# Performance work log

Hardware: AMD Instinct MI355X
Metric: run time of the kernel (lower is better)

The kernel has to match this reference:

```python
import jax, jax.numpy as jnp
import numpy as np

B, G, C = 16384, 7, 30  # batch, 7x7 grid, 2*5 box params + 20 classes


def setup_inputs() -> dict:
    key = jax.random.key(0)
    k1, k2 = jax.random.split(key)
    pred = jax.random.uniform(k1, (B, G, G, C), dtype=jnp.float32)
    labels = jax.random.uniform(k2, (B, G, G, C), dtype=jnp.float32)
    # channel 0 of labels is the object-presence indicator (==1 where a gt box exists)
    labels = labels.at[..., 0].set((labels[..., 0] > 0.7).astype(jnp.float32))
    return {"pred": pred, "labels": labels}


def _corners(box):
    # box channels: [conf, x, y, w, h]
    x, y, w, h = box[..., 1], box[..., 2], box[..., 3], box[..., 4]
    return x - 0.5 * w, x + 0.5 * w, y - 0.5 * h, y + 0.5 * h  # left,right,top,bottom


def _iou(b1, b2):
    l1, r1, t1, bt1 = _corners(b1)
    l2, r2, t2, bt2 = _corners(b2)
    in_h = jnp.minimum(bt1, bt2) - jnp.maximum(t1, t2)
    in_w = jnp.minimum(r1, r2) - jnp.maximum(l1, l2)
    inter = jnp.where((in_h < 0) | (in_w < 0), 0.0, in_h * in_w)
    area1 = (bt1 - t1) * (r1 - l1)
    area2 = (bt2 - t2) * (r2 - l2)
    return inter / (area1 + area2 - inter)


def reference(pred, labels):
    mask = labels[..., 0]                     # [B,7,7] object indicator (0/1)
    box1 = pred[..., 0:5]
    box2 = pred[..., 5:10]
    gt = labels[..., 0:5]
    iou1 = _iou(box1, gt)
    iou2 = _iou(box2, gt)
    best = iou1 >= iou2                       # responsible box per cell
    sel = jnp.where(best[..., None], box1, box2)
    iou_max = jnp.where(best, iou1, iou2)
    iou_min = jnp.where(best, iou2, iou1)
    center = 5.0 * ((sel[..., 1] - gt[..., 1]) ** 2 + (sel[..., 2] - gt[..., 2]) ** 2)
    wh = 5.0 * ((jnp.sqrt(sel[..., 3]) - jnp.sqrt(gt[..., 3])) ** 2
                + (jnp.sqrt(sel[..., 4]) - jnp.sqrt(gt[..., 4])) ** 2)
    cls = jnp.sum((pred[..., 10:] - labels[..., 10:]) ** 2, axis=-1)

    def msum(x):
        return jnp.sum(x * mask)

    # [center, wh, obj_conf, noobj_conf, classification]
    return jnp.stack([msum(center), msum(wh), msum(iou_max), msum(iou_min), msum(cls)])
```

## Files before the change

kernel.cpp:

```cpp
#include <hip/hip_runtime.h>

#define NCH 30
#define CPB 256
#define TPB 256

__device__ __forceinline__ float iou_f(float x1, float y1, float w1, float h1,
                                       float x2, float y2, float w2, float h2) {
    float l1 = x1 - 0.5f * w1, r1 = x1 + 0.5f * w1;
    float t1 = y1 - 0.5f * h1, b1 = y1 + 0.5f * h1;
    float l2 = x2 - 0.5f * w2, r2 = x2 + 0.5f * w2;
    float t2 = y2 - 0.5f * h2, b2 = y2 + 0.5f * h2;
    float in_h = fminf(b1, b2) - fmaxf(t1, t2);
    float in_w = fminf(r1, r2) - fmaxf(l1, l2);
    float inter = (in_h < 0.f || in_w < 0.f) ? 0.f : in_h * in_w;
    float a1 = (b1 - t1) * (r1 - l1);
    float a2 = (b2 - t2) * (r2 - l2);
    return inter / (a1 + a2 - inter);
}

__global__ __launch_bounds__(TPB) void yolo_loss(const float* __restrict__ pred,
                                                 const float* __restrict__ lab,
                                                 float* __restrict__ out,
                                                 int n_cells) {
    __shared__ float s_p[CPB * NCH];
    __shared__ float s_l[CPB * NCH];
    __shared__ float red[5][TPB / 64];

    const int tid = threadIdx.x;
    const size_t cell0 = (size_t)blockIdx.x * CPB;
    const size_t base = cell0 * NCH;
    const size_t total = (size_t)n_cells * NCH;

    const float4* gp = (const float4*)(pred + base);
    const float4* gl = (const float4*)(lab + base);
    float4* sp = (float4*)s_p;
    float4* sl = (float4*)s_l;
    const int nvec = CPB * NCH / 4;
    const size_t avail = (total > base) ? (total - base) : 0;
    const int nv = (int)((avail / 4) < (size_t)nvec ? (avail / 4) : (size_t)nvec);
    for (int i = tid; i < nv; i += TPB) {
        sp[i] = gp[i];
        sl[i] = gl[i];
    }
    __syncthreads();

    float v0 = 0.f, v1 = 0.f, v2 = 0.f, v3 = 0.f, v4 = 0.f;
    if (cell0 + (size_t)tid < (size_t)n_cells) {
        const float* cp = s_p + tid * NCH;
        const float* cl = s_l + tid * NCH;
        float mask = cl[0];
        float gx = cl[1], gy = cl[2], gw = cl[3], gh = cl[4];

        float i1 = iou_f(cp[1], cp[2], cp[3], cp[4], gx, gy, gw, gh);
        float i2 = iou_f(cp[6], cp[7], cp[8], cp[9], gx, gy, gw, gh);
        bool best = (i1 >= i2);
        float sx = best ? cp[1] : cp[6];
        float sy = best ? cp[2] : cp[7];
        float sw = best ? cp[3] : cp[8];
        float sh = best ? cp[4] : cp[9];
        float imax = best ? i1 : i2;
        float imin = best ? i2 : i1;

        float center = 5.f * ((sx - gx) * (sx - gx) + (sy - gy) * (sy - gy));
        float dw = sqrtf(sw) - sqrtf(gw);
        float dh = sqrtf(sh) - sqrtf(gh);
        float wh = 5.f * (dw * dw + dh * dh);

        float cls = 0.f;
#pragma unroll
        for (int c = 10; c < 30; ++c) {
            float d = cp[c] - cl[c];
            cls += d * d;
        }

        v0 = center * mask;
        v1 = wh * mask;
        v2 = imax * mask;
        v3 = imin * mask;
        v4 = cls * mask;
    }

#pragma unroll
    for (int off = 32; off > 0; off >>= 1) {
        v0 += __shfl_down(v0, off);
        v1 += __shfl_down(v1, off);
        v2 += __shfl_down(v2, off);
        v3 += __shfl_down(v3, off);
        v4 += __shfl_down(v4, off);
    }

    const int wave = tid >> 6;
    const int lane = tid & 63;
    if (lane == 0) {
        red[0][wave] = v0;
        red[1][wave] = v1;
        red[2][wave] = v2;
        red[3][wave] = v3;
        red[4][wave] = v4;
    }
    __syncthreads();

    if (tid < 5) {
        float s = 0.f;
#pragma unroll
        for (int w = 0; w < TPB / 64; ++w) s += red[tid][w];
        atomicAdd(&out[tid], s);
    }
}

extern "C" void kernel_launch(void* const* d_in, const int* in_sizes, int n_in,
                              void* d_out, int out_size, void* d_ws, size_t ws_size,
                              hipStream_t stream) {
    const float* pred = (const float*)d_in[0];
    const float* lab  = (const float*)d_in[1];
    float* out = (float*)d_out;

    const int n_cells = in_sizes[0] / NCH;
    const int grid = (n_cells + CPB - 1) / CPB;

    hipMemsetAsync(d_out, 0, out_size * sizeof(float), stream);
    hipLaunchKernelGGL(yolo_loss, dim3(grid), dim3(TPB), 0, stream,
                       pred, lab, out, n_cells);
}
```

Before: 217.7 us.

## Stage cells through shared memory in two half-size chunks to raise occupancy

The kernel now stages the block's 256 cells through shared memory in two chunks of 128 instead of all at once, which halves LDS use per block. It also adds a launch_bounds minimum of 5 blocks per SM. The goal is more resident blocks to hide memory latency. The cost is that only half the threads compute in each chunk, and there are extra barriers between the chunk loads.

```diff
diff --git a/kernel.cpp b/kernel.cpp
--- a/kernel.cpp
+++ b/kernel.cpp
@@ -1,6 +1,7 @@
 #include <hip/hip_runtime.h>
 
 #define NCH 30
+#define CHUNK 128
 #define CPB 256
 #define TPB 256
 
@@ -18,66 +19,78 @@
     return inter / (a1 + a2 - inter);
 }
 
-__global__ __launch_bounds__(TPB) void yolo_loss(const float* __restrict__ pred,
-                                                 const float* __restrict__ lab,
-                                                 float* __restrict__ out,
-                                                 int n_cells) {
-    __shared__ float s_p[CPB * NCH];
-    __shared__ float s_l[CPB * NCH];
+__global__ __launch_bounds__(TPB, 5) void yolo_loss(const float* __restrict__ pred,
+                                                    const float* __restrict__ lab,
+                                                    float* __restrict__ out,
+                                                    int n_cells) {
+    __shared__ float s_p[CHUNK * NCH];
+    __shared__ float s_l[CHUNK * NCH];
     __shared__ float red[5][TPB / 64];
 
     const int tid = threadIdx.x;
     const size_t cell0 = (size_t)blockIdx.x * CPB;
-    const size_t base = cell0 * NCH;
-    const size_t total = (size_t)n_cells * NCH;
-
-    const float4* gp = (const float4*)(pred + base);
-    const float4* gl = (const float4*)(lab + base);
-    float4* sp = (float4*)s_p;
-    float4* sl = (float4*)s_l;
-    const int nvec = CPB * NCH / 4;
-    const size_t avail = (total > base) ? (total - base) : 0;
-    const int nv = (int)((avail / 4) < (size_t)nvec ? (avail / 4) : (size_t)nvec);
-    for (int i = tid; i < nv; i += TPB) {
-        sp[i] = gp[i];
-        sl[i] = gl[i];
-    }
-    __syncthreads();
+    const size_t total_vec = (size_t)n_cells * NCH / 4;
 
     float v0 = 0.f, v1 = 0.f, v2 = 0.f, v3 = 0.f, v4 = 0.f;
-    if (cell0 + (size_t)tid < (size_t)n_cells) {
-        const float* cp = s_p + tid * NCH;
-        const float* cl = s_l + tid * NCH;
-        float mask = cl[0];
-        float gx = cl[1], gy = cl[2], gw = cl[3], gh = cl[4];
 
-        float i1 = iou_f(cp[1], cp[2], cp[3], cp[4], gx, gy, gw, gh);
-        float i2 = iou_f(cp[6], cp[7], cp[8], cp[9], gx, gy, gw, gh);
-        bool best = (i1 >= i2);
-        float sx = best ? cp[1] : cp[6];
-        float sy = best ? cp[2] : cp[7];
-        float sw = best ? cp[3] : cp[8];
-        float sh = best ? cp[4] : cp[9];
-        float imax = best ? i1 : i2;
-        float imin = best ? i2 : i1;
+    for (int chunk = 0; chunk < 2; ++chunk) {
+        const size_t cbase = cell0 + (size_t)chunk * CHUNK;
+        const size_t vbase = cbase * NCH / 4;
+        const float4* gp = (const float4*)pred + vbase;
+        const float4* gl = (const float4*)lab + vbase;
+        float4* sp = (float4*)s_p;
+        float4* sl = (float4*)s_l;
 
-        float center = 5.f * ((sx - gx) * (sx - gx) + (sy - gy) * (sy - gy));
-        float dw = sqrtf(sw) - sqrtf(gw);
-        float dh = sqrtf(sh) - sqrtf(gh);
-        float wh = 5.f * (dw * dw + dh * dh);
+        if (chunk) __syncthreads();
 
-        float cls = 0.f;
+        const int nvec = CHUNK * NCH / 4;
+        const size_t avail = (total_vec > vbase) ? (total_vec - vbase) : 0;
+        const int nv = (int)((avail < (size_t)nvec) ? avail : (size_t)nvec);
 #pragma unroll
-        for (int c = 10; c < 30; ++c) {
-            float d = cp[c] - cl[c];
-            cls += d * d;
+        for (int i = 0; i < nvec; i += TPB) {
+            int idx = i + tid;
+            if (idx < nv) {
+                sp[idx] = gp[idx];
+                sl[idx] = gl[idx];
+            }
         }
+        __syncthreads();
 
-        v0 = center * mask;
-        v1 = wh * mask;
-        v2 = imax * mask;
-        v3 = imin * mask;
-        v4 = cls * mask;
+        const int local = tid - chunk * CHUNK;
+        if (local >= 0 && local < CHUNK && cbase + (size_t)local < (size_t)n_cells) {
+            const float* cp = s_p + local * NCH;
+            const float* cl = s_l + local * NCH;
+            float mask = cl[0];
+            float gx = cl[1], gy = cl[2], gw = cl[3], gh = cl[4];
+
+            float i1 = iou_f(cp[1], cp[2], cp[3], cp[4], gx, gy, gw, gh);
+            float i2 = iou_f(cp[6], cp[7], cp[8], cp[9], gx, gy, gw, gh);
+            bool best = (i1 >= i2);
+            float sx = best ? cp[1] : cp[6];
+            float sy = best ? cp[2] : cp[7];
+            float sw = best ? cp[3] : cp[8];
+            float sh = best ? cp[4] : cp[9];
+            float imax = best ? i1 : i2;
+            float imin = best ? i2 : i1;
+
+            float center = 5.f * ((sx - gx) * (sx - gx) + (sy - gy) * (sy - gy));
+            float dw = sqrtf(sw) - sqrtf(gw);
+            float dh = sqrtf(sh) - sqrtf(gh);
+            float wh = 5.f * (dw * dw + dh * dh);
+
+            float cls = 0.f;
+#pragma unroll
+            for (int c = 10; c < 30; ++c) {
+                float d = cp[c] - cl[c];
+                cls += d * d;
+            }
+
+            v0 = center * mask;
+            v1 = wh * mask;
+            v2 = imax * mask;
+            v3 = imin * mask;
+            v4 = cls * mask;
+        }
     }
 
 #pragma unroll
```

After: 221.7 us. No clear change (+1.8%).
